# Optimization experiments

Measured on AMD Instinct MI355X. Metric: run time of the kernel, lower is better.

## Reference

```python
import jax, jax.numpy as jnp
import numpy as np

EPS = 1.1  # GIN epsilon from GINLayer(1.1, dim)
N_GIN = 4

def setup_inputs() -> dict:
    key = jax.random.key(0)
    ks = jax.random.split(key, 24)
    R, F_IN, H1, D = 1048576, 64, 256, 128
    N, E, B, A1, T = 100000, 1600000, 4096, 256, 16
    s = 0.05
    inp = {}
    inp['bulk'] = jax.random.normal(ks[0], (R, F_IN), dtype=jnp.float32)
    inp['seg_ids'] = jnp.sort(jax.random.randint(ks[1], (R,), 0, N))
    inp['edge_src'] = jax.random.randint(ks[2], (E,), 0, N)
    inp['edge_dst'] = jax.random.randint(ks[3], (E,), 0, N)
    inp['root_idx'] = jax.random.randint(ks[4], (B,), 0, N)
    inp['num_nodes'] = N
    # feature extractor: Linear(64,256)+ReLU, Linear(256,128)+ReLU
    inp['W1'] = jax.random.normal(ks[5], (F_IN, H1), dtype=jnp.float32) * s
    inp['b1'] = jnp.zeros((H1,), jnp.float32)
    inp['W2'] = jax.random.normal(ks[6], (H1, D), dtype=jnp.float32) * s
    inp['b2'] = jnp.zeros((D,), jnp.float32)
    # 4 GIN layers, dim D -> D
    inp['gin_W'] = jax.random.normal(ks[7], (N_GIN, D, D), dtype=jnp.float32) * s
    inp['gin_b'] = jnp.zeros((N_GIN, D), jnp.float32)
    # actor: Linear(128,256)+ReLU, Linear(256,16)+ReLU, Softmax
    inp['Wa1'] = jax.random.normal(ks[8], (D, A1), dtype=jnp.float32) * s
    inp['ba1'] = jnp.zeros((A1,), jnp.float32)
    inp['Wa2'] = jax.random.normal(ks[9], (A1, T), dtype=jnp.float32) * s
    inp['ba2'] = jnp.zeros((T,), jnp.float32)
    # critic: Linear(128,256)+ReLU, Linear(256,1)
    inp['Wc1'] = jax.random.normal(ks[10], (D, A1), dtype=jnp.float32) * s
    inp['bc1'] = jnp.zeros((A1,), jnp.float32)
    inp['Wc2'] = jax.random.normal(ks[11], (A1, 1), dtype=jnp.float32) * s
    inp['bc2'] = jnp.zeros((1,), jnp.float32)
    return inp

def reference(bulk, seg_ids, edge_src, edge_dst, root_idx, num_nodes,
              W1, b1, W2, b2, gin_W, gin_b, Wa1, ba1, Wa2, ba2, Wc1, bc1, Wc2, bc2):
    # feature extractor over all rows
    h = jax.nn.relu(bulk @ W1 + b1)
    h = jax.nn.relu(h @ W2 + b2)  # [R, D]
    # per-dataset mean aggregation (self.aggregator over split groups)
    sums = jax.ops.segment_sum(h, seg_ids, num_segments=num_nodes)
    counts = jax.ops.segment_sum(jnp.ones((h.shape[0],), h.dtype), seg_ids, num_segments=num_nodes)
    node_h = sums / jnp.maximum(counts, 1.0)[:, None]  # [N, D]
    # GIN message passing: h_v <- relu(W ((1+eps) h_v + sum_{child u} h_u) + b)
    for i in range(N_GIN):
        agg = jax.ops.segment_sum(node_h[edge_src], edge_dst, num_segments=num_nodes)
        node_h = jax.nn.relu(((1.0 + EPS) * node_h + agg) @ gin_W[i] + gin_b[i])
    X = node_h[root_idx]  # [B, D] current-node representations
    act = jax.nn.softmax(jax.nn.relu(jax.nn.relu(X @ Wa1 + ba1) @ Wa2 + ba2), axis=-1)
    crit = (jax.nn.relu(X @ Wc1 + bc1) @ Wc2 + bc2).squeeze(-1)
    return (act, crit)
```

## Files before the change

kernel.cpp:

```cpp
#include <hip/hip_runtime.h>
#include <math.h>

#define R_ROWS 1048576
#define F_IN   64
#define H1     256
#define D      128
#define NN     100000
#define NE     1600000
#define NB     4096
#define A1     256
#define NTOK   16
#define N_GIN  4
#define FE_ROWS 64

typedef short short8 __attribute__((ext_vector_type(8)));
typedef float f32x4  __attribute__((ext_vector_type(4)));
typedef unsigned int uintx4 __attribute__((ext_vector_type(4)));

__device__ __forceinline__ ushort f2bf(float x) {
    uint u = __builtin_bit_cast(uint, x);
    u += 0x7FFFu + ((u >> 16) & 1u);
    return (ushort)(u >> 16);
}
__device__ __forceinline__ float bf2f(ushort h) {
    uint u = ((uint)h) << 16;
    return __builtin_bit_cast(float, u);
}
__device__ __forceinline__ uint cvtpk(float lo, float hi) {
    uint r;
    asm("v_cvt_pk_bf16_f32 %0, %1, %2" : "=v"(r) : "v"(lo), "v"(hi));
    return r;
}
__device__ __forceinline__ float lo16f(uint p) { return __builtin_bit_cast(float, p << 16); }
__device__ __forceinline__ float hi16f(uint p) { return __builtin_bit_cast(float, p & 0xFFFF0000u); }

__device__ __forceinline__ f32x4 mm(short8 a, short8 b, f32x4 c) {
    return __builtin_amdgcn_mfma_f32_16x16x32_bf16(a, b, c, 0, 0, 0);
}
__device__ __forceinline__ void acc_add(f32x4& L, f32x4& H, const uintx4 p) {
    L[0] += lo16f(p[0]); H[0] += hi16f(p[0]);
    L[1] += lo16f(p[1]); H[1] += hi16f(p[1]);
    L[2] += lo16f(p[2]); H[2] += hi16f(p[2]);
    L[3] += lo16f(p[3]); H[3] += hi16f(p[3]);
}

__device__ __forceinline__ void pack_one(const float* __restrict__ W, int Ndim,
                                         int f, int lane, ushort* __restrict__ out)
{
    const int NTn = Ndim >> 4;
    const int kt = f / NTn, nt = f - kt * NTn;
    const int k0 = kt * 32 + (lane >> 4) * 8;
    const int n = nt * 16 + (lane & 15);
    uintx4 Hv, Lv;
    #pragma unroll
    for (int jj = 0; jj < 4; ++jj) {
        const float x0 = W[(k0 + 2 * jj) * Ndim + n];
        const float x1 = W[(k0 + 2 * jj + 1) * Ndim + n];
        const ushort h0 = f2bf(x0), l0 = f2bf(x0 - bf2f(h0));
        const ushort h1u = f2bf(x1), l1 = f2bf(x1 - bf2f(h1u));
        Hv[jj] = (uint)h0 | ((uint)h1u << 16);
        Lv[jj] = (uint)l0 | ((uint)l1 << 16);
    }
    *reinterpret_cast<uintx4*>(&out[((f * 2 + 0) * 64 + lane) * 8]) = Hv;
    *reinterpret_cast<uintx4*>(&out[((f * 2 + 1) * 64 + lane) * 8]) = Lv;
}

__global__ __launch_bounds__(256) void pack_weights(
    const float* __restrict__ W, int Ndim, int nfrag, ushort* __restrict__ out)
{
    const int id = blockIdx.x * 256 + threadIdx.x;
    const int f = id >> 6, lane = id & 63;
    if (f >= nfrag) return;
    pack_one(W, Ndim, f, lane, out);
}

__global__ __launch_bounds__(256) void pack_gin(
    const float* __restrict__ ginW, ushort* __restrict__ out)
{
    const int l = blockIdx.y;
    const int id = blockIdx.x * 256 + threadIdx.x;
    const int f = id >> 6, lane = id & 63;
    if (f >= 32) return;
    pack_one(ginW + (long)l * D * D, D, f, lane, out + (long)l * 32768);
}

__global__ __launch_bounds__(256, 4) void fe_mfma(
    const float* __restrict__ bulk, const int* __restrict__ seg,
    const ushort* __restrict__ W1p, const float* __restrict__ b1,
    const ushort* __restrict__ W2p, const float* __restrict__ b2,
    float* __restrict__ sums)
{
    __shared__ __align__(16) uint smem_u[10240];
    char* Ab  = (char*)smem_u;
    char* h1b = Ab + 8192;
    float* h2 = (float*)smem_u;

    const int t = threadIdx.x;
    const int lane = t & 63;
    const int w = t >> 6;
    const long r0 = (long)blockIdx.x * FE_ROWS;

    #pragma unroll
    for (int i = 0; i < 4; ++i) {
        const int gid = t + i * 256;
        const int row = gid >> 4;
        const int c4 = (gid & 15) * 4;
        const float4 v = *reinterpret_cast<const float4*>(&bulk[(r0 + row) * F_IN + c4]);
        uint2 pk; pk.x = cvtpk(v.x, v.y); pk.y = cvtpk(v.z, v.w);
        const int byteoff = row * 128 + ((c4 * 2) ^ ((row & 7) << 4));
        *reinterpret_cast<uint2*>(Ab + byteoff) = pk;
    }
    __syncthreads();

    const f32x4 zz = {0.f, 0.f, 0.f, 0.f};
    f32x4 acc1[4][4];
    #pragma unroll
    for (int mtl = 0; mtl < 4; ++mtl)
        #pragma unroll
        for (int ntb = 0; ntb < 4; ++ntb) acc1[mtl][ntb] = zz;

    #pragma unroll
    for (int kt = 0; kt < 2; ++kt) {
        short8 aw[4][2];
        #pragma unroll
        for (int mtl = 0; mtl < 4; ++mtl)
            #pragma unroll
            for (int p = 0; p < 2; ++p) {
                const int f = kt * 16 + (w * 4 + mtl);
                aw[mtl][p] = *reinterpret_cast<const short8*>(&W1p[((f * 2 + p) * 64 + lane) * 8]);
            }
        short8 bh[4];
        #pragma unroll
        for (int ntb = 0; ntb < 4; ++ntb) {
            const int row = ntb * 16 + (lane & 15);
            const int k0 = kt * 32 + (lane >> 4) * 8;
            bh[ntb] = *reinterpret_cast<const short8*>(Ab + (row * 128 + ((k0 * 2) ^ ((row & 7) << 4))));
        }
        #pragma unroll
        for (int mtl = 0; mtl < 4; ++mtl)
            #pragma unroll
            for (int ntb = 0; ntb < 4; ++ntb) {
                acc1[mtl][ntb] = mm(aw[mtl][0], bh[ntb], acc1[mtl][ntb]);
                acc1[mtl][ntb] = mm(aw[mtl][1], bh[ntb], acc1[mtl][ntb]);
            }
    }

    #pragma unroll
    for (int mtl = 0; mtl < 4; ++mtl) {
        const int hcb = w * 64 + mtl * 16 + (lane >> 4) * 4;
        const float4 bv = *reinterpret_cast<const float4*>(&b1[hcb]);
        #pragma unroll
        for (int ntb = 0; ntb < 4; ++ntb) {
            const int hr = (lane & 15) + ntb * 16;
            const float v0 = fmaxf(acc1[mtl][ntb][0] + bv.x, 0.f);
            const float v1 = fmaxf(acc1[mtl][ntb][1] + bv.y, 0.f);
            const float v2 = fmaxf(acc1[mtl][ntb][2] + bv.z, 0.f);
            const float v3 = fmaxf(acc1[mtl][ntb][3] + bv.w, 0.f);
            uint2 pk; pk.x = cvtpk(v0, v1); pk.y = cvtpk(v2, v3);
            const int byteoff = (hr * 512 + hcb * 2) ^ ((hr & 7) << 4);
            *reinterpret_cast<uint2*>(h1b + byteoff) = pk;
        }
    }
    __syncthreads();

    float b2v[2];
    #pragma unroll
    for (int ntl = 0; ntl < 2; ++ntl) b2v[ntl] = b2[w * 32 + ntl * 16 + (lane & 15)];
    f32x4 acc2[4][2];
    #pragma unroll
    for (int mt = 0; mt < 4; ++mt) { acc2[mt][0] = zz; acc2[mt][1] = zz; }

    #pragma unroll
    for (int kt = 0; kt < 8; ++kt) {
        short8 bw2[2][2];
        #pragma unroll
        for (int ntl = 0; ntl < 2; ++ntl)
            #pragma unroll
            for (int p = 0; p < 2; ++p) {
                const int f = kt * 8 + (w * 2 + ntl);
                bw2[ntl][p] = *reinterpret_cast<const short8*>(&W2p[((f * 2 + p) * 64 + lane) * 8]);
            }
        short8 ah[4];
        #pragma unroll
        for (int mt = 0; mt < 4; ++mt) {
            const int row = mt * 16 + (lane & 15);
            const int k0 = kt * 32 + (lane >> 4) * 8;
            ah[mt] = *reinterpret_cast<const short8*>(h1b + ((row * 512 + k0 * 2) ^ ((row & 7) << 4)));
        }
        #pragma unroll
        for (int mt = 0; mt < 4; ++mt)
            #pragma unroll
            for (int ntl = 0; ntl < 2; ++ntl) {
                acc2[mt][ntl] = mm(ah[mt], bw2[ntl][0], acc2[mt][ntl]);
                acc2[mt][ntl] = mm(ah[mt], bw2[ntl][1], acc2[mt][ntl]);
            }
    }
    __syncthreads();

    #pragma unroll
    for (int mt = 0; mt < 4; ++mt)
        #pragma unroll
        for (int ntl = 0; ntl < 2; ++ntl)
            #pragma unroll
            for (int r = 0; r < 4; ++r) {
                const int row = mt * 16 + (lane >> 4) * 4 + r;
                const int col = w * 32 + ntl * 16 + (lane & 15);
                h2[row * 132 + col] = fmaxf(acc2[mt][ntl][r] + b2v[ntl], 0.f);
            }
    __syncthreads();

    {
        const int g = t >> 7;
        const int c = t & 127;
        const int base = g * 32;
        const long rb = r0 + base;
        const int prev = (rb == 0) ? -1 : seg[rb - 1];
        const int nxt = (rb + 32 >= R_ROWS) ? -1 : seg[rb + 32];
        int cur = seg[rb];
        float run = 0.f;
        int runstart = 0;
        #pragma unroll 1
        for (int r = 0; r < 32; ++r) {
            const int s = seg[rb + r];
            if (s != cur) {
                if (runstart != 0 || cur != prev) sums[(long)cur * D + c] = run;
                else atomicAdd(&sums[(long)cur * D + c], run);
                cur = s; run = 0.f; runstart = r;
            }
            run += h2[(base + r) * 132 + c];
        }
        if ((runstart != 0 || cur != prev) && cur != nxt) sums[(long)cur * D + c] = run;
        else atomicAdd(&sums[(long)cur * D + c], run);
    }
}

__global__ __launch_bounds__(256) void start_kernel(const int* __restrict__ seg,
                                                    int* __restrict__ start)
{
    const int n = blockIdx.x * 256 + threadIdx.x;
    if (n > NN) return;
    int lo = 0, hi = R_ROWS;
    #pragma unroll 1
    while (lo < hi) {
        const int mid = (lo + hi) >> 1;
        if (seg[mid] < n) lo = mid + 1; else hi = mid;
    }
    start[n] = lo;
}

__global__ __launch_bounds__(256) void divide_bf(
    const float* __restrict__ sums, const int* __restrict__ start,
    uint* __restrict__ hbf)
{
    const long i = (long)blockIdx.x * 256 + threadIdx.x;
    if (i < (long)NN * 64) {
        const int n = (int)(i >> 6), u = (int)(i & 63);
        const int cA = (u & 15) + (u >> 4) * 32;
        const float inv = 1.f / fmaxf((float)(start[n + 1] - start[n]), 1.f);
        const float vA = sums[(long)n * D + cA] * inv;
        const float vB = sums[(long)n * D + cA + 16] * inv;
        hbf[i] = cvtpk(vA, vB);
    }
}

__global__ __launch_bounds__(256) void hist_kernel(const int* __restrict__ edst,
                                                   int* __restrict__ deg)
{
    const int e = blockIdx.x * 256 + threadIdx.x;
    if (e < NE) atomicAdd(&deg[edst[e]], 1);
}

#define SCHUNK 2048
__global__ __launch_bounds__(256) void scan_reduce(const int* __restrict__ deg,
                                                   int* __restrict__ partials, int n)
{
    __shared__ int sdata[256];
    const int b = blockIdx.x, t = threadIdx.x;
    const int base = b * SCHUNK;
    int sum = 0;
    for (int i = t; i < SCHUNK; i += 256) {
        const int idx = base + i;
        sum += (idx < n) ? deg[idx] : 0;
    }
    sdata[t] = sum; __syncthreads();
    for (int s = 128; s > 0; s >>= 1) {
        if (t < s) sdata[t] += sdata[t + s];
        __syncthreads();
    }
    if (t == 0) partials[b] = sdata[0];
}

__global__ void scan_partials(int* partials, int nb)
{
    if (threadIdx.x == 0) {
        int acc = 0;
        for (int i = 0; i < nb; ++i) { const int v = partials[i]; partials[i] = acc; acc += v; }
    }
}

__global__ __launch_bounds__(256) void scan_write(const int* __restrict__ deg,
                                                  const int* __restrict__ partials,
                                                  int* __restrict__ offsets, int n)
{
    __shared__ int sdata[256];
    const int b = blockIdx.x, t = threadIdx.x;
    const int base = b * SCHUNK;
    int loc[8]; int s = 0;
    #pragma unroll
    for (int j = 0; j < 8; ++j) {
        const int idx = base + t * 8 + j;
        const int v = (idx < n) ? deg[idx] : 0;
        loc[j] = s; s += v;
    }
    sdata[t] = s; __syncthreads();
    for (int d = 1; d < 256; d <<= 1) {
        const int v = (t >= d) ? sdata[t - d] : 0;
        __syncthreads();
        sdata[t] += v;
        __syncthreads();
    }
    const int excl = (t == 0) ? 0 : sdata[t - 1];
    const int tbase = partials[b] + excl;
    #pragma unroll
    for (int j = 0; j < 8; ++j) {
        const int idx = base + t * 8 + j;
        if (idx < n) offsets[idx] = tbase + loc[j];
    }
}

__global__ __launch_bounds__(256) void scatter_edges(const int* __restrict__ esrc,
                                                     const int* __restrict__ edst,
                                                     int* __restrict__ cursor,
                                                     int* __restrict__ csr_src)
{
    const int e = blockIdx.x * 256 + threadIdx.x;
    if (e < NE) {
        const int d = edst[e];
        const int p = atomicAdd(&cursor[d], 1);
        csr_src[p] = esrc[e];
    }
}

__global__ __launch_bounds__(256) void mark_kernel(
    const int* __restrict__ root, const int* __restrict__ offsets,
    const int* __restrict__ deg, const int* __restrict__ csr,
    int* __restrict__ mark)
{
    const int b = blockIdx.x * 256 + threadIdx.x;
    if (b < NB) {
        const int n = root[b];
        mark[n] = 1;
        const int off = offsets[n], dg = deg[n];
        for (int j = 0; j < dg; ++j) mark[csr[off + j]] = 1;
    }
}

__global__ __launch_bounds__(256) void compact_kernel(
    const int* __restrict__ mark, int* __restrict__ list, int* __restrict__ cnt)
{
    const int n = blockIdx.x * 256 + threadIdx.x;
    if (n < NN && mark[n]) {
        const int p = atomicAdd(cnt, 1);
        list[p] = n;
    }
}

template<int MODE>
__global__ __launch_bounds__(256, 8) void gin_kernel(
    const uint* __restrict__ hbf, const int* __restrict__ offsets,
    const int* __restrict__ deg, const int* __restrict__ csr,
    const ushort* __restrict__ Wp, const float* __restrict__ bvec,
    uint* __restrict__ outbuf,
    const int* __restrict__ list, const int* __restrict__ cnt,
    const int* __restrict__ root)
{
    __shared__ __align__(16) char ylds[64 * 256];
    __shared__ int nid[64];
    const int t = threadIdx.x, lane = t & 63, w = t >> 6;
    const int q = lane >> 4, m = lane & 15;
    const int r0 = blockIdx.x * 64;
    const int CNT = (MODE == 1) ? cnt[0] : 0;
    if (MODE == 1 && r0 >= CNT) return;

    #pragma unroll 1
    for (int i = 0; i < 16; ++i) {
        const int row = w * 16 + i;
        int n = -1;
        if (MODE == 0) {
            const int nn = r0 + row;
            if (nn < NN) n = nn;
        } else if (MODE == 1) {
            const int idx = r0 + row;
            if (idx < CNT) n = list[idx];
        } else {
            n = root[r0 + row];
        }
        if (MODE == 1 && lane == 0) nid[row] = n;
        f32x4 accL = {0.f, 0.f, 0.f, 0.f};
        f32x4 accH = {0.f, 0.f, 0.f, 0.f};
        if (n >= 0) {
            const uintx4 sp = *reinterpret_cast<const uintx4*>(&hbf[(long)n * 64 + 4 * m]);
            const float sc = (q == 0) ? 2.1f : 0.f;
            accL[0] = sc * lo16f(sp[0]); accH[0] = sc * hi16f(sp[0]);
            accL[1] = sc * lo16f(sp[1]); accH[1] = sc * hi16f(sp[1]);
            accL[2] = sc * lo16f(sp[2]); accH[2] = sc * hi16f(sp[2]);
            accL[3] = sc * lo16f(sp[3]); accH[3] = sc * hi16f(sp[3]);
            const int off = offsets[n];
            const int dg = deg[n];
            const int dg4 = dg >> 2;
            int jj = 0;
            for (; jj + 4 <= dg4; jj += 4) {
                const int b = off + 4 * jj + q;
                const int s0 = csr[b], s1 = csr[b + 4], s2 = csr[b + 8], s3 = csr[b + 12];
                const uintx4 p0 = *reinterpret_cast<const uintx4*>(&hbf[(long)s0 * 64 + 4 * m]);
                const uintx4 p1 = *reinterpret_cast<const uintx4*>(&hbf[(long)s1 * 64 + 4 * m]);
                const uintx4 p2 = *reinterpret_cast<const uintx4*>(&hbf[(long)s2 * 64 + 4 * m]);
                const uintx4 p3 = *reinterpret_cast<const uintx4*>(&hbf[(long)s3 * 64 + 4 * m]);
                acc_add(accL, accH, p0);
                acc_add(accL, accH, p1);
                acc_add(accL, accH, p2);
                acc_add(accL, accH, p3);
            }
            for (; jj < dg4; ++jj) {
                const int s = csr[off + 4 * jj + q];
                const uintx4 p = *reinterpret_cast<const uintx4*>(&hbf[(long)s * 64 + 4 * m]);
                acc_add(accL, accH, p);
            }
            for (int j = dg4 * 4; j < dg; ++j) {
                if (q == (j & 3)) {
                    const int s = csr[off + j];
                    const uintx4 p = *reinterpret_cast<const uintx4*>(&hbf[(long)s * 64 + 4 * m]);
                    acc_add(accL, accH, p);
                }
            }
        }
        #pragma unroll
        for (int e = 0; e < 4; ++e) {
            accL[e] += __shfl_xor(accL[e], 16);
            accH[e] += __shfl_xor(accH[e], 16);
            accL[e] += __shfl_xor(accL[e], 32);
            accH[e] += __shfl_xor(accH[e], 32);
        }
        const float vA = (q == 0) ? accL[0] : (q == 1) ? accL[1] : (q == 2) ? accL[2] : accL[3];
        const float vB = (q == 0) ? accH[0] : (q == 1) ? accH[1] : (q == 2) ? accH[2] : accH[3];
        const int u = 4 * m + q;
        const int cA = (u & 15) + (u >> 4) * 32;
        const int swz = (row & 7) << 4;
        const uint pk = cvtpk(vA, vB);
        *reinterpret_cast<ushort*>(ylds + ((row * 256 + cA * 2) ^ swz)) = (ushort)pk;
        *reinterpret_cast<ushort*>(ylds + ((row * 256 + (cA + 16) * 2) ^ swz)) = (ushort)(pk >> 16);
    }

    short8 bw0[2][2];
    #pragma unroll
    for (int ntl = 0; ntl < 2; ++ntl)
        #pragma unroll
        for (int p = 0; p < 2; ++p) {
            const int f = w * 2 + ntl;
            bw0[ntl][p] = *reinterpret_cast<const short8*>(&Wp[((f * 2 + p) * 64 + lane) * 8]);
        }
    __syncthreads();

    const f32x4 zz = {0.f, 0.f, 0.f, 0.f};
    f32x4 acc[4][2];
    #pragma unroll
    for (int mt = 0; mt < 4; ++mt) { acc[mt][0] = zz; acc[mt][1] = zz; }

    #pragma unroll
    for (int kt = 0; kt < 4; ++kt) {
        short8 bw[2][2];
        if (kt == 0) {
            #pragma unroll
            for (int ntl = 0; ntl < 2; ++ntl)
                #pragma unroll
                for (int p = 0; p < 2; ++p) bw[ntl][p] = bw0[ntl][p];
        } else {
            #pragma unroll
            for (int ntl = 0; ntl < 2; ++ntl)
                #pragma unroll
                for (int p = 0; p < 2; ++p) {
                    const int f = kt * 8 + (w * 2 + ntl);
                    bw[ntl][p] = *reinterpret_cast<const short8*>(&Wp[((f * 2 + p) * 64 + lane) * 8]);
                }
        }
        #pragma unroll
        for (int mt = 0; mt < 4; ++mt) {
            const int row = mt * 16 + m;
            const int k0 = kt * 32 + q * 8;
            const short8 ah = *reinterpret_cast<const short8*>(
                ylds + ((row * 256 + k0 * 2) ^ ((row & 7) << 4)));
            acc[mt][0] = mm(ah, bw[0][0], acc[mt][0]);
            acc[mt][0] = mm(ah, bw[0][1], acc[mt][0]);
            acc[mt][1] = mm(ah, bw[1][0], acc[mt][1]);
            acc[mt][1] = mm(ah, bw[1][1], acc[mt][1]);
        }
    }

    const float bv0 = bvec[w * 32 + m];
    const float bv1 = bvec[w * 32 + 16 + m];
    #pragma unroll
    for (int mt = 0; mt < 4; ++mt)
        #pragma unroll
        for (int r = 0; r < 4; ++r) {
            const int grow_row = mt * 16 + q * 4 + r;
            const float v0 = fmaxf(acc[mt][0][r] + bv0, 0.f);
            const float v1 = fmaxf(acc[mt][1][r] + bv1, 0.f);
            const uint pk = cvtpk(v0, v1);
            if (MODE == 0) {
                const long nout = r0 + grow_row;
                if (nout < NN) outbuf[nout * 64 + w * 16 + m] = pk;
            } else if (MODE == 1) {
                if (r0 + grow_row < CNT) {
                    const long nout = nid[grow_row];
                    outbuf[nout * 64 + w * 16 + m] = pk;
                }
            } else {
                outbuf[(long)(r0 + grow_row) * 64 + w * 16 + m] = pk;
            }
        }
}

__global__ __launch_bounds__(256) void head_kernel(
    const uint* __restrict__ Xbf, const int* __restrict__ root,
    const float* __restrict__ Wa1, const float* __restrict__ ba1,
    const float* __restrict__ Wa2, const float* __restrict__ ba2,
    const float* __restrict__ Wc1, const float* __restrict__ bc1,
    const float* __restrict__ Wc2, const float* __restrict__ bc2,
    float* __restrict__ out_act, float* __restrict__ out_crit)
{
    __shared__ float X[D];
    __shared__ float a1[A1];
    __shared__ float red[256];
    __shared__ float logits[NTOK];
    const int t = threadIdx.x;
    const int bi = blockIdx.x;
    if (t < 64) {
        const uint p = Xbf[(long)bi * 64 + t];
        const int cA = (t & 15) + (t >> 4) * 32;
        X[cA] = lo16f(p);
        X[cA + 16] = hi16f(p);
    }
    __syncthreads();

    float acc = ba1[t];
    #pragma unroll
    for (int k = 0; k < D; k += 4) {
        const float4 xv = *reinterpret_cast<const float4*>(&X[k]);
        acc = fmaf(xv.x, Wa1[(k + 0) * A1 + t], acc);
        acc = fmaf(xv.y, Wa1[(k + 1) * A1 + t], acc);
        acc = fmaf(xv.z, Wa1[(k + 2) * A1 + t], acc);
        acc = fmaf(xv.w, Wa1[(k + 3) * A1 + t], acc);
    }
    a1[t] = fmaxf(acc, 0.f);
    __syncthreads();

    const int j = t & 15, p = t >> 4;
    float pa = 0.f;
    #pragma unroll
    for (int k = 0; k < 16; ++k) {
        const int kk = p * 16 + k;
        pa = fmaf(a1[kk], Wa2[kk * NTOK + j], pa);
    }
    red[j * 16 + p] = pa;
    __syncthreads();
    if (t < NTOK) {
        float s = 0.f;
        #pragma unroll
        for (int p2 = 0; p2 < 16; ++p2) s += red[t * 16 + p2];
        logits[t] = fmaxf(s + ba2[t], 0.f);
    }
    __syncthreads();
    if (t < NTOK) {
        float mx = -1e30f;
        #pragma unroll
        for (int i = 0; i < NTOK; ++i) mx = fmaxf(mx, logits[i]);
        red[t] = expf(logits[t] - mx);
    }
    __syncthreads();
    if (t < NTOK) {
        float s = 0.f;
        #pragma unroll
        for (int i = 0; i < NTOK; ++i) s += red[i];
        out_act[(long)bi * NTOK + t] = red[t] / s;
    }
    __syncthreads();

    float accc = bc1[t];
    #pragma unroll
    for (int k = 0; k < D; k += 4) {
        const float4 xv = *reinterpret_cast<const float4*>(&X[k]);
        accc = fmaf(xv.x, Wc1[(k + 0) * A1 + t], accc);
        accc = fmaf(xv.y, Wc1[(k + 1) * A1 + t], accc);
        accc = fmaf(xv.z, Wc1[(k + 2) * A1 + t], accc);
        accc = fmaf(xv.w, Wc1[(k + 3) * A1 + t], accc);
    }
    red[t] = fmaxf(accc, 0.f) * Wc2[t];
    __syncthreads();
    for (int s = 128; s > 0; s >>= 1) {
        if (t < s) red[t] += red[t + s];
        __syncthreads();
    }
    if (t == 0) out_crit[bi] = red[0] + bc2[0];
}

extern "C" void kernel_launch(void* const* d_in, const int* in_sizes, int n_in,
                              void* d_out, int out_size, void* d_ws, size_t ws_size,
                              hipStream_t stream)
{
    const float* bulk = (const float*)d_in[0];
    const int*   seg  = (const int*)d_in[1];
    const int*   esrc = (const int*)d_in[2];
    const int*   edst = (const int*)d_in[3];
    const int*   root = (const int*)d_in[4];
    const float* W1   = (const float*)d_in[6];
    const float* b1   = (const float*)d_in[7];
    const float* W2   = (const float*)d_in[8];
    const float* b2   = (const float*)d_in[9];
    const float* ginW = (const float*)d_in[10];
    const float* ginb = (const float*)d_in[11];
    const float* Wa1  = (const float*)d_in[12];
    const float* ba1  = (const float*)d_in[13];
    const float* Wa2  = (const float*)d_in[14];
    const float* ba2  = (const float*)d_in[15];
    const float* Wc1  = (const float*)d_in[16];
    const float* bc1  = (const float*)d_in[17];
    const float* Wc2  = (const float*)d_in[18];
    const float* bc2  = (const float*)d_in[19];

    char* ws = (char*)d_ws;
    ushort* W1p = (ushort*)ws;
    ushort* W2p = W1p + 32768;
    float* sums    = (float*)(ws + 196608);
    uint*  hbfA    = (uint*)(sums + (long)NN * D);
    uint*  hbfB    = hbfA + (long)NN * 64;
    int*   start   = (int*)(hbfB + (long)NN * 64);
    int*   deg     = start + (NN + 4);
    int*   offsets = deg + NN;
    int*   cursor  = offsets + NN;
    int*   partials= cursor + NN;
    int*   csr     = partials + 256;
    int*   mark    = csr + NE;
    int*   list    = mark + NN;
    int*   cnt     = list + NN;
    uint*  Xbf     = (uint*)(cnt + 4);
    ushort* Gp     = (ushort*)cursor;

    pack_weights<<<8, 256, 0, stream>>>(W1, H1, 32, W1p);
    pack_weights<<<16, 256, 0, stream>>>(W2, D, 64, W2p);

    hipMemsetAsync(sums, 0, (long)NN * D * sizeof(float), stream);
    hipMemsetAsync(deg, 0, NN * sizeof(int), stream);
    hipMemsetAsync(mark, 0, NN * sizeof(int), stream);
    hipMemsetAsync(cnt, 0, sizeof(int), stream);

    fe_mfma<<<R_ROWS / FE_ROWS, 256, 0, stream>>>(bulk, seg, W1p, b1, W2p, b2, sums);
    start_kernel<<<(NN + 256) / 256, 256, 0, stream>>>(seg, start);
    divide_bf<<<((long)NN * 64 + 255) / 256, 256, 0, stream>>>(sums, start, hbfA);

    hist_kernel<<<(NE + 255) / 256, 256, 0, stream>>>(edst, deg);
    const int nchunks = (NN + SCHUNK - 1) / SCHUNK;
    scan_reduce<<<nchunks, 256, 0, stream>>>(deg, partials, NN);
    scan_partials<<<1, 64, 0, stream>>>(partials, nchunks);
    scan_write<<<nchunks, 256, 0, stream>>>(deg, partials, offsets, NN);
    hipMemcpyAsync(cursor, offsets, NN * sizeof(int), hipMemcpyDeviceToDevice, stream);
    scatter_edges<<<(NE + 255) / 256, 256, 0, stream>>>(esrc, edst, cursor, csr);

    mark_kernel<<<(NB + 255) / 256, 256, 0, stream>>>(root, offsets, deg, csr, mark);
    compact_kernel<<<(NN + 255) / 256, 256, 0, stream>>>(mark, list, cnt);

    pack_gin<<<dim3(8, 4), 256, 0, stream>>>(ginW, Gp);

    const int full_grid = (NN + 63) / 64;
    gin_kernel<0><<<full_grid, 256, 0, stream>>>(hbfA, offsets, deg, csr,
        Gp + 0L * 32768, ginb + 0L * D, hbfB, list, cnt, root);
    gin_kernel<0><<<full_grid, 256, 0, stream>>>(hbfB, offsets, deg, csr,
        Gp + 1L * 32768, ginb + 1L * D, hbfA, list, cnt, root);
    gin_kernel<1><<<full_grid, 256, 0, stream>>>(hbfA, offsets, deg, csr,
        Gp + 2L * 32768, ginb + 2L * D, hbfB, list, cnt, root);
    gin_kernel<2><<<NB / 64, 256, 0, stream>>>(hbfB, offsets, deg, csr,
        Gp + 3L * 32768, ginb + 3L * D, Xbf, list, cnt, root);

    head_kernel<<<NB, 256, 0, stream>>>(Xbf, root, Wa1, ba1, Wa2, ba2,
                                        Wc1, bc1, Wc2, bc2,
                                        (float*)d_out, (float*)d_out + (long)NB * NTOK);
}
```

Baseline: 845.1 us.

## Merge weight packing and zeroing kernels, fuse scan steps, process two GIN rows per wave

Combines the three weight-packing launches and three memsets into one pack_all kernel, folds the partial-sum scan into scan_write via a wave reduction, and writes the cursor copy directly, which removes a device memcpy. The GIN gather now has each half-wave handle its own node with two edge lanes per node, replacing four edge lanes for a single node. The goal is fewer launches and better lane use on low-degree nodes, at the cost of less memory-level parallelism per node. Gp moves out of the cursor region, since the cursor is now live before packing happens.

```diff
diff --git a/kernel.cpp b/kernel.cpp
--- a/kernel.cpp
+++ b/kernel.cpp
@@ -65,23 +65,33 @@
     *reinterpret_cast<uintx4*>(&out[((f * 2 + 1) * 64 + lane) * 8]) = Lv;
 }
 
-__global__ __launch_bounds__(256) void pack_weights(
-    const float* __restrict__ W, int Ndim, int nfrag, ushort* __restrict__ out)
-{
-    const int id = blockIdx.x * 256 + threadIdx.x;
-    const int f = id >> 6, lane = id & 63;
-    if (f >= nfrag) return;
-    pack_one(W, Ndim, f, lane, out);
-}
-
-__global__ __launch_bounds__(256) void pack_gin(
-    const float* __restrict__ ginW, ushort* __restrict__ out)
-{
-    const int l = blockIdx.y;
-    const int id = blockIdx.x * 256 + threadIdx.x;
-    const int f = id >> 6, lane = id & 63;
-    if (f >= 32) return;
-    pack_one(ginW + (long)l * D * D, D, f, lane, out + (long)l * 32768);
+__global__ __launch_bounds__(256) void pack_all(
+    const float* __restrict__ W1, const float* __restrict__ W2,
+    const float* __restrict__ ginW,
+    ushort* __restrict__ W1p, ushort* __restrict__ W2p, ushort* __restrict__ Gp,
+    int* __restrict__ deg, int* __restrict__ mark, int* __restrict__ cnt)
+{
+    const int bid = blockIdx.x;
+    if (bid < 56) {
+        const int fid = bid * 4 + (threadIdx.x >> 6);
+        const int lane = threadIdx.x & 63;
+        if (fid < 32) pack_one(W1, H1, fid, lane, W1p);
+        else if (fid < 96) pack_one(W2, D, fid - 32, lane, W2p);
+        else {
+            const int l = (fid - 96) >> 5;
+            pack_one(ginW + (long)l * D * D, D, (fid - 96) & 31, lane, Gp + (long)l * 32768);
+        }
+    } else {
+        const int zb = bid - 56;
+        const int idx0 = (zb * 256 + threadIdx.x) * 4;
+        #pragma unroll
+        for (int k = 0; k < 4; ++k) {
+            const int idx = idx0 + k;
+            if (idx < NN) deg[idx] = 0;
+            else if (idx < 2 * NN) mark[idx - NN] = 0;
+        }
+        if (bid == 56 && threadIdx.x == 0) cnt[0] = 0;
+    }
 }
 
 __global__ __launch_bounds__(256, 4) void fe_mfma(
@@ -290,20 +300,21 @@
     if (t == 0) partials[b] = sdata[0];
 }
 
-__global__ void scan_partials(int* partials, int nb)
-{
-    if (threadIdx.x == 0) {
-        int acc = 0;
-        for (int i = 0; i < nb; ++i) { const int v = partials[i]; partials[i] = acc; acc += v; }
-    }
-}
-
 __global__ __launch_bounds__(256) void scan_write(const int* __restrict__ deg,
                                                   const int* __restrict__ partials,
-                                                  int* __restrict__ offsets, int n)
+                                                  int nchunks,
+                                                  int* __restrict__ offsets,
+                                                  int* __restrict__ cursor, int n)
 {
     __shared__ int sdata[256];
+    __shared__ int base_sh;
     const int b = blockIdx.x, t = threadIdx.x;
+    if (t < 64) {
+        int v = (t < b && t < nchunks) ? partials[t] : 0;
+        #pragma unroll
+        for (int d2 = 1; d2 < 64; d2 <<= 1) v += __shfl_xor(v, d2);
+        if (t == 0) base_sh = v;
+    }
     const int base = b * SCHUNK;
     int loc[8]; int s = 0;
     #pragma unroll
@@ -320,11 +331,15 @@
         __syncthreads();
     }
     const int excl = (t == 0) ? 0 : sdata[t - 1];
-    const int tbase = partials[b] + excl;
+    const int tbase = base_sh + excl;
     #pragma unroll
     for (int j = 0; j < 8; ++j) {
         const int idx = base + t * 8 + j;
-        if (idx < n) offsets[idx] = tbase + loc[j];
+        if (idx < n) {
+            const int o = tbase + loc[j];
+            offsets[idx] = o;
+            cursor[idx] = o;
+        }
     }
 }
 
@@ -377,14 +392,17 @@
     __shared__ __align__(16) char ylds[64 * 256];
     __shared__ int nid[64];
     const int t = threadIdx.x, lane = t & 63, w = t >> 6;
-    const int q = lane >> 4, m = lane & 15;
+    const int h = lane >> 5;
+    const int q2 = (lane >> 4) & 1;
+    const int m = lane & 15;
+    const int q = lane >> 4;
     const int r0 = blockIdx.x * 64;
     const int CNT = (MODE == 1) ? cnt[0] : 0;
     if (MODE == 1 && r0 >= CNT) return;
 
     #pragma unroll 1
-    for (int i = 0; i < 16; ++i) {
-        const int row = w * 16 + i;
+    for (int i = 0; i < 8; ++i) {
+        const int row = w * 16 + i * 2 + h;
         int n = -1;
         if (MODE == 0) {
             const int nn = r0 + row;
@@ -395,23 +413,23 @@
         } else {
             n = root[r0 + row];
         }
-        if (MODE == 1 && lane == 0) nid[row] = n;
+        if (MODE == 1 && (lane & 31) == 0) nid[row] = n;
         f32x4 accL = {0.f, 0.f, 0.f, 0.f};
         f32x4 accH = {0.f, 0.f, 0.f, 0.f};
         if (n >= 0) {
             const uintx4 sp = *reinterpret_cast<const uintx4*>(&hbf[(long)n * 64 + 4 * m]);
-            const float sc = (q == 0) ? 2.1f : 0.f;
+            const float sc = (q2 == 0) ? 2.1f : 0.f;
             accL[0] = sc * lo16f(sp[0]); accH[0] = sc * hi16f(sp[0]);
             accL[1] = sc * lo16f(sp[1]); accH[1] = sc * hi16f(sp[1]);
             accL[2] = sc * lo16f(sp[2]); accH[2] = sc * hi16f(sp[2]);
             accL[3] = sc * lo16f(sp[3]); accH[3] = sc * hi16f(sp[3]);
             const int off = offsets[n];
             const int dg = deg[n];
-            const int dg4 = dg >> 2;
+            const int dg2 = dg >> 1;
             int jj = 0;
-            for (; jj + 4 <= dg4; jj += 4) {
-                const int b = off + 4 * jj + q;
-                const int s0 = csr[b], s1 = csr[b + 4], s2 = csr[b + 8], s3 = csr[b + 12];
+            for (; jj + 4 <= dg2; jj += 4) {
+                const int b0 = off + 2 * jj + q2;
+                const int s0 = csr[b0], s1 = csr[b0 + 2], s2 = csr[b0 + 4], s3 = csr[b0 + 6];
                 const uintx4 p0 = *reinterpret_cast<const uintx4*>(&hbf[(long)s0 * 64 + 4 * m]);
                 const uintx4 p1 = *reinterpret_cast<const uintx4*>(&hbf[(long)s1 * 64 + 4 * m]);
                 const uintx4 p2 = *reinterpret_cast<const uintx4*>(&hbf[(long)s2 * 64 + 4 * m]);
@@ -421,34 +439,31 @@
                 acc_add(accL, accH, p2);
                 acc_add(accL, accH, p3);
             }
-            for (; jj < dg4; ++jj) {
-                const int s = csr[off + 4 * jj + q];
+            for (; jj < dg2; ++jj) {
+                const int s = csr[off + 2 * jj + q2];
                 const uintx4 p = *reinterpret_cast<const uintx4*>(&hbf[(long)s * 64 + 4 * m]);
                 acc_add(accL, accH, p);
             }
-            for (int j = dg4 * 4; j < dg; ++j) {
-                if (q == (j & 3)) {
-                    const int s = csr[off + j];
-                    const uintx4 p = *reinterpret_cast<const uintx4*>(&hbf[(long)s * 64 + 4 * m]);
-                    acc_add(accL, accH, p);
-                }
+            if ((dg & 1) && q2 == 0) {
+                const int s = csr[off + dg - 1];
+                const uintx4 p = *reinterpret_cast<const uintx4*>(&hbf[(long)s * 64 + 4 * m]);
+                acc_add(accL, accH, p);
             }
         }
         #pragma unroll
         for (int e = 0; e < 4; ++e) {
             accL[e] += __shfl_xor(accL[e], 16);
             accH[e] += __shfl_xor(accH[e], 16);
-            accL[e] += __shfl_xor(accL[e], 32);
-            accH[e] += __shfl_xor(accH[e], 32);
-        }
-        const float vA = (q == 0) ? accL[0] : (q == 1) ? accL[1] : (q == 2) ? accL[2] : accL[3];
-        const float vB = (q == 0) ? accH[0] : (q == 1) ? accH[1] : (q == 2) ? accH[2] : accH[3];
-        const int u = 4 * m + q;
-        const int cA = (u & 15) + (u >> 4) * 32;
+        }
         const int swz = (row & 7) << 4;
-        const uint pk = cvtpk(vA, vB);
-        *reinterpret_cast<ushort*>(ylds + ((row * 256 + cA * 2) ^ swz)) = (ushort)pk;
-        *reinterpret_cast<ushort*>(ylds + ((row * 256 + (cA + 16) * 2) ^ swz)) = (ushort)(pk >> 16);
+        #pragma unroll
+        for (int e = 0; e < 2; ++e) {
+            const int u = 4 * m + 2 * q2 + e;
+            const int cA = (u & 15) + (u >> 4) * 32;
+            const uint pk = cvtpk(accL[2 * q2 + e], accH[2 * q2 + e]);
+            *reinterpret_cast<ushort*>(ylds + ((row * 256 + cA * 2) ^ swz)) = (ushort)pk;
+            *reinterpret_cast<ushort*>(ylds + ((row * 256 + (cA + 16) * 2) ^ swz)) = (ushort)(pk >> 16);
+        }
     }
 
     short8 bw0[2][2];
@@ -643,15 +658,11 @@
     int*   list    = mark + NN;
     int*   cnt     = list + NN;
     uint*  Xbf     = (uint*)(cnt + 4);
-    ushort* Gp     = (ushort*)cursor;
-
-    pack_weights<<<8, 256, 0, stream>>>(W1, H1, 32, W1p);
-    pack_weights<<<16, 256, 0, stream>>>(W2, D, 64, W2p);
+    ushort* Gp     = (ushort*)(Xbf + (long)NB * 64);
 
     hipMemsetAsync(sums, 0, (long)NN * D * sizeof(float), stream);
-    hipMemsetAsync(deg, 0, NN * sizeof(int), stream);
-    hipMemsetAsync(mark, 0, NN * sizeof(int), stream);
-    hipMemsetAsync(cnt, 0, sizeof(int), stream);
+
+    pack_all<<<252, 256, 0, stream>>>(W1, W2, ginW, W1p, W2p, Gp, deg, mark, cnt);
 
     fe_mfma<<<R_ROWS / FE_ROWS, 256, 0, stream>>>(bulk, seg, W1p, b1, W2p, b2, sums);
     start_kernel<<<(NN + 256) / 256, 256, 0, stream>>>(seg, start);
@@ -660,15 +671,11 @@
     hist_kernel<<<(NE + 255) / 256, 256, 0, stream>>>(edst, deg);
     const int nchunks = (NN + SCHUNK - 1) / SCHUNK;
     scan_reduce<<<nchunks, 256, 0, stream>>>(deg, partials, NN);
-    scan_partials<<<1, 64, 0, stream>>>(partials, nchunks);
-    scan_write<<<nchunks, 256, 0, stream>>>(deg, partials, offsets, NN);
-    hipMemcpyAsync(cursor, offsets, NN * sizeof(int), hipMemcpyDeviceToDevice, stream);
+    scan_write<<<nchunks, 256, 0, stream>>>(deg, partials, nchunks, offsets, cursor, NN);
     scatter_edges<<<(NE + 255) / 256, 256, 0, stream>>>(esrc, edst, cursor, csr);
 
     mark_kernel<<<(NB + 255) / 256, 256, 0, stream>>>(root, offsets, deg, csr, mark);
     compact_kernel<<<(NN + 255) / 256, 256, 0, stream>>>(mark, list, cnt);
-
-    pack_gin<<<dim3(8, 4), 256, 0, stream>>>(ginW, Gp);
 
     const int full_grid = (NN + 63) / 64;
     gin_kernel<0><<<full_grid, 256, 0, stream>>>(hbfA, offsets, deg, csr,
```

New measurement: 775.2 us. 1.09x faster.
